# Performance work log

Measured on AMD Instinct MI355X. Metric: run time of the kernel, lower is better.

## Reference

```python
import jax, jax.numpy as jnp
import numpy as np
import math

B, T, C = 2, 2048, 1024
H = 16
D = C // H

def setup_inputs() -> dict:
    key = jax.random.key(0)
    k1, k2, k3, k4, k5 = jax.random.split(key, 5)
    scale = 0.02
    return {
        "x": jax.random.normal(k1, (B, T, C), dtype=jnp.float32),
        "w_attn": jax.random.normal(k2, (3 * C, C), dtype=jnp.float32) * scale,
        "b_attn": jax.random.normal(k3, (3 * C,), dtype=jnp.float32) * scale,
        "w_proj": jax.random.normal(k4, (C, C), dtype=jnp.float32) * scale,
        "b_proj": jax.random.normal(k5, (C,), dtype=jnp.float32) * scale,
    }

def reference(x, w_attn, b_attn, w_proj, b_proj):
    b, t, c = x.shape
    # c_attn: torch Linear -> x @ W.T + b, output [b, t, 3c]
    qkv = jnp.einsum('btc,fc->btf', x, w_attn) + b_attn
    # einops 'b t (a h d) -> a b h t d' with a=3, h=H
    qkv = qkv.reshape(b, t, 3, H, D).transpose(2, 0, 3, 1, 4)
    q, k, v = qkv[0], qkv[1], qkv[2]  # each [b, h, t, d]
    att = jnp.einsum('bhtd,bhsd->bhts', q, k) * (1.0 / math.sqrt(D))
    # causal mask: positions s > t are masked
    mask = jnp.tril(jnp.ones((t, t), dtype=bool))
    att = jnp.where(mask[None, None, :, :], att, jnp.float32(-jnp.inf))
    att = jax.nn.softmax(att, axis=-1)
    y = jnp.einsum('bhts,bhsd->bhtd', att, v)  # [b, h, t, d]
    y = y.transpose(0, 2, 1, 3).reshape(b, t, c)
    return jnp.einsum('btc,fc->btf', y, w_proj) + b_proj
```

## Files before the change

### kernel.cpp

```cpp
#include <hip/hip_runtime.h>
#include <stdint.h>

typedef unsigned short u16;
typedef __attribute__((ext_vector_type(8))) __bf16 bvec8;
typedef __attribute__((ext_vector_type(4))) float f32x4;

__device__ __forceinline__ u16 f32_to_bf16(float f) {
    uint32_t u = __float_as_uint(f);
    u += 0x7fffu + ((u >> 16) & 1u);
    return (u16)(u >> 16);
}

__device__ __forceinline__ void gl2lds16(const u16* g, u16* l) {
    void* gnc = const_cast<void*>((const void*)g);
    __builtin_amdgcn_global_load_lds(
        (__attribute__((address_space(1))) uint32_t*)gnc,
        (__attribute__((address_space(3))) uint32_t*)((void*)l),
        16, 0, 0);
}

__global__ __launch_bounds__(256) void cvt3(
    const float* __restrict__ a, int na4, const float* __restrict__ b, int nb4,
    const float* __restrict__ c, int nc4,
    u16* __restrict__ oa, u16* __restrict__ ob, u16* __restrict__ oc)
{
    int i = blockIdx.x * 256 + threadIdx.x;
    const float* src; u16* dst; int off;
    if (i < na4)             { src = a; dst = oa; off = i; }
    else if (i < na4 + nb4)  { src = b; dst = ob; off = i - na4; }
    else if (i < na4 + nb4 + nc4) { src = c; dst = oc; off = i - na4 - nb4; }
    else return;
    float4 v = ((const float4*)src)[off];
    ushort4 o;
    o.x = f32_to_bf16(v.x); o.y = f32_to_bf16(v.y);
    o.z = f32_to_bf16(v.z); o.w = f32_to_bf16(v.w);
    ((ushort4*)dst)[off] = o;
}

template <int BNt, bool OUT_BF16>
__global__ __launch_bounds__(256) void gemm_bt_bias(
    const u16* __restrict__ A, const u16* __restrict__ B,
    const float* __restrict__ bias, void* __restrict__ Cv,
    int M, int N, int K)
{
    constexpr int NT = BNt / 32;
    __shared__ __attribute__((aligned(16))) u16 As[2][128 * 32];
    __shared__ __attribute__((aligned(16))) u16 Bs[2][BNt * 32];

    const int tid = threadIdx.x, wave = tid >> 6, lane = tid & 63;
    const int col = lane & 15, quad = lane >> 4;
    const int m0 = blockIdx.y * 128, n0 = blockIdx.x * BNt;
    const int wm = (wave >> 1) * 64, wn = (wave & 1) * (BNt / 2);
    const int srow = lane >> 2, schunk = lane & 3;
    const int fs = (srow & 3) ^ ((srow >> 2) & 3);
    const int sc = (schunk ^ fs) * 8;
    const int xsw = (quad ^ (col & 3) ^ ((col >> 2) & 3)) * 8;

    const u16* Ag = A + (size_t)(m0 + wave * 32) * K;
    const u16* Bg = B + (size_t)(n0 + wave * (BNt == 128 ? 32 : 16)) * K;

    f32x4 acc[4][NT];
#pragma unroll
    for (int i = 0; i < 4; i++)
#pragma unroll
        for (int j = 0; j < NT; j++) acc[i][j] = f32x4{0.f, 0.f, 0.f, 0.f};

    auto stage = [&](int bb, int k0) {
        gl2lds16(Ag + (size_t)(srow)      * K + k0 + sc, &As[bb][(wave * 2 + 0) * 512]);
        gl2lds16(Ag + (size_t)(16 + srow) * K + k0 + sc, &As[bb][(wave * 2 + 1) * 512]);
        if constexpr (BNt == 128) {
            gl2lds16(Bg + (size_t)(srow)      * K + k0 + sc, &Bs[bb][(wave * 2 + 0) * 512]);
            gl2lds16(Bg + (size_t)(16 + srow) * K + k0 + sc, &Bs[bb][(wave * 2 + 1) * 512]);
        } else {
            gl2lds16(Bg + (size_t)(srow)      * K + k0 + sc, &Bs[bb][wave * 512]);
        }
    };

    stage(0, 0);
    const int NS = K / 32;

    for (int t = 0; t < NS; ++t) {
        const int cur = t & 1;
        if (t + 1 < NS) {
            stage(cur ^ 1, (t + 1) * 32);
            if constexpr (BNt == 128) asm volatile("s_waitcnt vmcnt(4)" ::: "memory");
            else                      asm volatile("s_waitcnt vmcnt(3)" ::: "memory");
        } else {
            asm volatile("s_waitcnt vmcnt(0)" ::: "memory");
        }
        asm volatile("s_barrier" ::: "memory");

        bvec8 af[4], bfv[NT];
#pragma unroll
        for (int mt = 0; mt < 4; mt++)  af[mt]  = *(const bvec8*)&As[cur][(wm + mt * 16 + col) * 32 + xsw];
#pragma unroll
        for (int nt = 0; nt < NT; nt++) bfv[nt] = *(const bvec8*)&Bs[cur][(wn + nt * 16 + col) * 32 + xsw];
#pragma unroll
        for (int mt = 0; mt < 4; mt++)
#pragma unroll
            for (int nt = 0; nt < NT; nt++)
                acc[mt][nt] = __builtin_amdgcn_mfma_f32_16x16x32_bf16(af[mt], bfv[nt], acc[mt][nt], 0, 0, 0);

        asm volatile("s_barrier" ::: "memory");
    }

#pragma unroll
    for (int mt = 0; mt < 4; mt++) {
#pragma unroll
        for (int r = 0; r < 4; r++) {
            const int m = m0 + wm + mt * 16 + quad * 4 + r;
#pragma unroll
            for (int nt = 0; nt < NT; nt++) {
                const int n = n0 + wn + nt * 16 + col;
                float v = acc[mt][nt][r] + bias[n];
                if (OUT_BF16) ((u16*)Cv)[(size_t)m * N + n] = f32_to_bf16(v);
                else          ((float*)Cv)[(size_t)m * N + n] = v;
            }
        }
    }
}

__global__ __launch_bounds__(256) void transpose_v(const u16* __restrict__ qkv,
                                                   u16* __restrict__ vT)
{
    __shared__ u16 Ts[64 * 74];
    const int tid = threadIdx.x;
    const int t0 = blockIdx.x * 64, h = blockIdx.y, b = blockIdx.z;
    const u16* src = qkv + (size_t)b * 2048 * 3072 + 2048 + h * 64;
#pragma unroll
    for (int k2 = 0; k2 < 2; k2++) {
        int c = k2 * 256 + tid, tl = c >> 3, ch = c & 7;
        *(uint4*)&Ts[tl * 74 + ch * 8] = *(const uint4*)(src + (size_t)(t0 + tl) * 3072 + ch * 8);
    }
    __syncthreads();
    u16* dst = vT + (size_t)((b * 16 + h) * 64) * 2048;
#pragma unroll
    for (int k2 = 0; k2 < 2; k2++) {
        int c = k2 * 256 + tid, d = c >> 3, tch = c & 7;
        u16 tmp[8];
#pragma unroll
        for (int j2 = 0; j2 < 8; j2++) tmp[j2] = Ts[(tch * 8 + j2) * 74 + d];
        *(uint4*)&dst[(size_t)d * 2048 + t0 + tch * 8] = *(const uint4*)tmp;
    }
}

__global__ __launch_bounds__(256) void attn_kernel(const u16* __restrict__ qkv,
                                                   const u16* __restrict__ vT,
                                                   u16* __restrict__ Y)
{
    __shared__ __attribute__((aligned(16))) u16 Ks[2][64 * 64];
    __shared__ __attribute__((aligned(16))) u16 Vs[2][64 * 64];

    const int tid = threadIdx.x, wave = tid >> 6, lane = tid & 63;
    const int col = lane & 15, quad = lane >> 4;

    const int g = blockIdx.x;
    const int b = g >> 4, h = g & 15;
    const int y0 = blockIdx.y & 7, s = blockIdx.y >> 3;
    const int qt = (s & 1) ? ((s & 2) ? 8 + y0 : y0)
                           : ((s & 2) ? 23 - y0 : 31 - y0);
    const int q0 = qt * 64;

    const u16* qb = qkv + (size_t)b * 2048 * 3072;
    const u16* vb = vT + (size_t)g * 64 * 2048;

    const int c0 = wave * 64 + lane, c1 = 256 + c0;
    const int r0 = c0 >> 3, p0 = c0 & 7, r1 = c1 >> 3, p1 = c1 & 7;
    const int sw0 = (p0 ^ (r0 & 7)) * 8, sw1 = (p1 ^ (r1 & 7)) * 8;
    const int tau0 = (r0 & 32) | ((r0 & 12) << 1) | ((r0 & 16) >> 2) | (r0 & 3);
    const int tau1 = (r1 & 32) | ((r1 & 12) << 1) | ((r1 & 16) >> 2) | (r1 & 3);

    const int q8 = quad * 8;
    const int qit = wave * 16 + col;
    const int qrow = wave * 16 + col;

    gl2lds16(qb + (size_t)(tau0) * 3072 + 1024 + h * 64 + sw0, &Ks[0][wave * 512]);
    gl2lds16(qb + (size_t)(tau1) * 3072 + 1024 + h * 64 + sw1, &Ks[0][2048 + wave * 512]);
    gl2lds16(vb + (size_t)r0 * 2048 + sw0, &Vs[0][wave * 512]);
    gl2lds16(vb + (size_t)r1 * 2048 + sw1, &Vs[0][2048 + wave * 512]);

    const u16* qrp = qb + (size_t)(q0 + qrow) * 3072 + h * 64;
    bvec8 qf0 = *(const bvec8*)(qrp + quad * 8);
    bvec8 qf1 = *(const bvec8*)(qrp + 32 + quad * 8);

    float l_acc = 0.f;
    f32x4 o[4];
#pragma unroll
    for (int d = 0; d < 4; d++) o[d] = f32x4{0.f, 0.f, 0.f, 0.f};

    for (int kt = 0; kt <= qt; ++kt) {
        const int cur = kt & 1;
        if (kt < qt) {
            const int s0n = (kt + 1) * 64;
            const int nb2 = cur ^ 1;
            gl2lds16(qb + (size_t)(s0n + tau0) * 3072 + 1024 + h * 64 + sw0, &Ks[nb2][wave * 512]);
            gl2lds16(qb + (size_t)(s0n + tau1) * 3072 + 1024 + h * 64 + sw1, &Ks[nb2][2048 + wave * 512]);
            gl2lds16(vb + (size_t)r0 * 2048 + s0n + sw0, &Vs[nb2][wave * 512]);
            gl2lds16(vb + (size_t)r1 * 2048 + s0n + sw1, &Vs[nb2][2048 + wave * 512]);
            asm volatile("s_waitcnt vmcnt(4)" ::: "memory");
        } else {
            asm volatile("s_waitcnt vmcnt(0)" ::: "memory");
        }
        asm volatile("s_barrier" ::: "memory");

        f32x4 sv[4];
#pragma unroll
        for (int nt = 0; nt < 4; nt++) {
            const int krow = nt * 16 + col;
            bvec8 kf0 = *(const bvec8*)&Ks[cur][krow * 64 + ((quad       ^ (krow & 7)) * 8)];
            bvec8 kf1 = *(const bvec8*)&Ks[cur][krow * 64 + (((4 + quad) ^ (krow & 7)) * 8)];
            sv[nt] = f32x4{0.f, 0.f, 0.f, 0.f};
            sv[nt] = __builtin_amdgcn_mfma_f32_16x16x32_bf16(kf0, qf0, sv[nt], 0, 0, 0);
            sv[nt] = __builtin_amdgcn_mfma_f32_16x16x32_bf16(kf1, qf1, sv[nt], 0, 0, 0);
        }

        const bool diag = (kt == qt);
        bvec8 pbv[2];
#pragma unroll
        for (int nt = 0; nt < 4; nt++) {
#pragma unroll
            for (int r = 0; r < 4; r++) {
                float p = __builtin_amdgcn_exp2f(sv[nt][r] * 0.1803368801111244f);
                const int klog = 32 * (nt >> 1) + q8 + 4 * (nt & 1) + r;
                if (diag && klog > qit) p = 0.f;
                l_acc += p;
                pbv[nt >> 1][(nt & 1) * 4 + r] = (__bf16)p;
            }
        }

#pragma unroll
        for (int ks = 0; ks < 2; ks++) {
#pragma unroll
            for (int d = 0; d < 4; d++) {
                const int vrow = d * 16 + col;
                bvec8 vf = *(const bvec8*)&Vs[cur][vrow * 64 + (((ks * 4 + quad) ^ (vrow & 7)) * 8)];
                o[d] = __builtin_amdgcn_mfma_f32_16x16x32_bf16(pbv[ks], vf, o[d], 0, 0, 0);
            }
        }
        asm volatile("s_barrier" ::: "memory");
    }

    float l = l_acc;
    l += __shfl_xor(l, 16);
    l += __shfl_xor(l, 32);
#pragma unroll
    for (int r = 0; r < 4; r++) {
        const float lr = __shfl(l, quad * 4 + r);
        const float inv = 1.0f / lr;
        const int t = q0 + wave * 16 + quad * 4 + r;
#pragma unroll
        for (int d = 0; d < 4; d++)
            Y[(size_t)(b * 2048 + t) * 1024 + h * 64 + d * 16 + col] =
                f32_to_bf16(o[d][r] * inv);
    }
}

extern "C" void kernel_launch(void* const* d_in, const int* in_sizes, int n_in,
                              void* d_out, int out_size, void* d_ws, size_t ws_size,
                              hipStream_t stream) {
    const float* x      = (const float*)d_in[0];
    const float* w_attn = (const float*)d_in[1];
    const float* b_attn = (const float*)d_in[2];
    const float* w_proj = (const float*)d_in[3];
    const float* b_proj = (const float*)d_in[4];
    float* out = (float*)d_out;

    u16* xb  = (u16*)d_ws;
    u16* wab = xb  + (size_t)4096 * 1024;
    u16* wpb = wab + (size_t)3072 * 1024;
    u16* qkv = wpb + (size_t)1024 * 1024;
    u16* y   = qkv + (size_t)4096 * 3072;
    u16* vT  = xb;

    const int na4 = 4096 * 1024 / 4, nb4 = 3072 * 1024 / 4, nc4 = 1024 * 1024 / 4;
    cvt3<<<(na4 + nb4 + nc4 + 255) / 256, 256, 0, stream>>>(
        x, na4, w_attn, nb4, w_proj, nc4, xb, wab, wpb);

    dim3 g1(3072 / 128, 4096 / 128);
    gemm_bt_bias<128, true><<<g1, 256, 0, stream>>>(xb, wab, b_attn, qkv, 4096, 3072, 1024);

    dim3 gt(32, 16, 2);
    transpose_v<<<gt, 256, 0, stream>>>(qkv, vT);

    dim3 g2(32, 32, 1);
    attn_kernel<<<g2, 256, 0, stream>>>(qkv, vT, y);

    dim3 g3(1024 / 64, 4096 / 128);
    gemm_bt_bias<64, false><<<g3, 256, 0, stream>>>(y, wpb, b_proj, out, 4096, 1024, 1024);
}
```

Before: 179.8 us.

## Halve attention block to two waves each handling 32 query rows

The attention kernel now runs with 128 threads, and each of its two waves handles two 16-row query tiles (A and B) instead of one. Every K and V fragment read from LDS feeds twice as many MFMAs, so LDS read traffic per unit of compute is halved. Each thread now issues four async global-to-LDS loads per K and V tile instead of two, and the waitcnt was raised to match. The cost is more registers per thread and fewer waves per block, which may reduce latency hiding across the barrier-synchronised loop.

```diff
diff --git a/kernel.cpp b/kernel.cpp
--- a/kernel.cpp
+++ b/kernel.cpp
@@ -144,7 +144,7 @@
     }
 }
 
-__global__ __launch_bounds__(256) void attn_kernel(const u16* __restrict__ qkv,
+__global__ __launch_bounds__(128) void attn_kernel(const u16* __restrict__ qkv,
                                                    const u16* __restrict__ vT,
                                                    u16* __restrict__ Y)
 {
@@ -164,67 +164,84 @@
     const u16* qb = qkv + (size_t)b * 2048 * 3072;
     const u16* vb = vT + (size_t)g * 64 * 2048;
 
-    const int c0 = wave * 64 + lane, c1 = 256 + c0;
-    const int r0 = c0 >> 3, p0 = c0 & 7, r1 = c1 >> 3, p1 = c1 & 7;
-    const int sw0 = (p0 ^ (r0 & 7)) * 8, sw1 = (p1 ^ (r1 & 7)) * 8;
-    const int tau0 = (r0 & 32) | ((r0 & 12) << 1) | ((r0 & 16) >> 2) | (r0 & 3);
-    const int tau1 = (r1 & 32) | ((r1 & 12) << 1) | ((r1 & 16) >> 2) | (r1 & 3);
-
-    const int q8 = quad * 8;
-    const int qit = wave * 16 + col;
-    const int qrow = wave * 16 + col;
-
-    gl2lds16(qb + (size_t)(tau0) * 3072 + 1024 + h * 64 + sw0, &Ks[0][wave * 512]);
-    gl2lds16(qb + (size_t)(tau1) * 3072 + 1024 + h * 64 + sw1, &Ks[0][2048 + wave * 512]);
-    gl2lds16(vb + (size_t)r0 * 2048 + sw0, &Vs[0][wave * 512]);
-    gl2lds16(vb + (size_t)r1 * 2048 + sw1, &Vs[0][2048 + wave * 512]);
-
-    const u16* qrp = qb + (size_t)(q0 + qrow) * 3072 + h * 64;
-    bvec8 qf0 = *(const bvec8*)(qrp + quad * 8);
-    bvec8 qf1 = *(const bvec8*)(qrp + 32 + quad * 8);
-
-    float l_acc = 0.f;
-    f32x4 o[4];
-#pragma unroll
-    for (int d = 0; d < 4; d++) o[d] = f32x4{0.f, 0.f, 0.f, 0.f};
+    int rj[4], swj[4], tj[4];
+#pragma unroll
+    for (int j = 0; j < 4; j++) {
+        const int c = j * 128 + tid, r = c >> 3, p = c & 7;
+        rj[j] = r;
+        swj[j] = (p ^ (r & 7)) * 8;
+        tj[j] = (r & 32) | ((r & 12) << 1) | ((r & 16) >> 2) | (r & 3);
+    }
+
+    auto stageK = [&](int bb, int s0) {
+#pragma unroll
+        for (int j = 0; j < 4; j++)
+            gl2lds16(qb + (size_t)(s0 + tj[j]) * 3072 + 1024 + h * 64 + swj[j],
+                     &Ks[bb][j * 1024 + wave * 512]);
+    };
+    auto stageV = [&](int bb, int s0) {
+#pragma unroll
+        for (int j = 0; j < 4; j++)
+            gl2lds16(vb + (size_t)rj[j] * 2048 + s0 + swj[j],
+                     &Vs[bb][j * 1024 + wave * 512]);
+    };
+
+    stageK(0, 0);
+    stageV(0, 0);
+
+    const int qitA = wave * 32 + col, qitB = qitA + 16;
+    const u16* qpA = qb + (size_t)(q0 + qitA) * 3072 + h * 64;
+    const u16* qpB = qpA + (size_t)16 * 3072;
+    bvec8 qfA0 = *(const bvec8*)(qpA + quad * 8);
+    bvec8 qfA1 = *(const bvec8*)(qpA + 32 + quad * 8);
+    bvec8 qfB0 = *(const bvec8*)(qpB + quad * 8);
+    bvec8 qfB1 = *(const bvec8*)(qpB + 32 + quad * 8);
+
+    float lA = 0.f, lB = 0.f;
+    f32x4 oA[4], oB[4];
+#pragma unroll
+    for (int d = 0; d < 4; d++) { oA[d] = f32x4{0.f, 0.f, 0.f, 0.f}; oB[d] = f32x4{0.f, 0.f, 0.f, 0.f}; }
 
     for (int kt = 0; kt <= qt; ++kt) {
         const int cur = kt & 1;
         if (kt < qt) {
-            const int s0n = (kt + 1) * 64;
-            const int nb2 = cur ^ 1;
-            gl2lds16(qb + (size_t)(s0n + tau0) * 3072 + 1024 + h * 64 + sw0, &Ks[nb2][wave * 512]);
-            gl2lds16(qb + (size_t)(s0n + tau1) * 3072 + 1024 + h * 64 + sw1, &Ks[nb2][2048 + wave * 512]);
-            gl2lds16(vb + (size_t)r0 * 2048 + s0n + sw0, &Vs[nb2][wave * 512]);
-            gl2lds16(vb + (size_t)r1 * 2048 + s0n + sw1, &Vs[nb2][2048 + wave * 512]);
-            asm volatile("s_waitcnt vmcnt(4)" ::: "memory");
+            stageK(cur ^ 1, (kt + 1) * 64);
+            stageV(cur ^ 1, (kt + 1) * 64);
+            asm volatile("s_waitcnt vmcnt(8)" ::: "memory");
         } else {
             asm volatile("s_waitcnt vmcnt(0)" ::: "memory");
         }
         asm volatile("s_barrier" ::: "memory");
 
-        f32x4 sv[4];
+        f32x4 svA[4], svB[4];
 #pragma unroll
         for (int nt = 0; nt < 4; nt++) {
             const int krow = nt * 16 + col;
             bvec8 kf0 = *(const bvec8*)&Ks[cur][krow * 64 + ((quad       ^ (krow & 7)) * 8)];
             bvec8 kf1 = *(const bvec8*)&Ks[cur][krow * 64 + (((4 + quad) ^ (krow & 7)) * 8)];
-            sv[nt] = f32x4{0.f, 0.f, 0.f, 0.f};
-            sv[nt] = __builtin_amdgcn_mfma_f32_16x16x32_bf16(kf0, qf0, sv[nt], 0, 0, 0);
-            sv[nt] = __builtin_amdgcn_mfma_f32_16x16x32_bf16(kf1, qf1, sv[nt], 0, 0, 0);
+            svA[nt] = f32x4{0.f, 0.f, 0.f, 0.f};
+            svA[nt] = __builtin_amdgcn_mfma_f32_16x16x32_bf16(kf0, qfA0, svA[nt], 0, 0, 0);
+            svA[nt] = __builtin_amdgcn_mfma_f32_16x16x32_bf16(kf1, qfA1, svA[nt], 0, 0, 0);
+            svB[nt] = f32x4{0.f, 0.f, 0.f, 0.f};
+            svB[nt] = __builtin_amdgcn_mfma_f32_16x16x32_bf16(kf0, qfB0, svB[nt], 0, 0, 0);
+            svB[nt] = __builtin_amdgcn_mfma_f32_16x16x32_bf16(kf1, qfB1, svB[nt], 0, 0, 0);
         }
 
         const bool diag = (kt == qt);
-        bvec8 pbv[2];
+        bvec8 pbvA[2], pbvB[2];
 #pragma unroll
         for (int nt = 0; nt < 4; nt++) {
 #pragma unroll
             for (int r = 0; r < 4; r++) {
-                float p = __builtin_amdgcn_exp2f(sv[nt][r] * 0.1803368801111244f);
-                const int klog = 32 * (nt >> 1) + q8 + 4 * (nt & 1) + r;
-                if (diag && klog > qit) p = 0.f;
-                l_acc += p;
-                pbv[nt >> 1][(nt & 1) * 4 + r] = (__bf16)p;
+                const int klog = 32 * (nt >> 1) + quad * 8 + 4 * (nt & 1) + r;
+                float pA = __builtin_amdgcn_exp2f(svA[nt][r] * 0.1803368801111244f);
+                if (diag && klog > qitA) pA = 0.f;
+                lA += pA;
+                pbvA[nt >> 1][(nt & 1) * 4 + r] = (__bf16)pA;
+                float pB = __builtin_amdgcn_exp2f(svB[nt][r] * 0.1803368801111244f);
+                if (diag && klog > qitB) pB = 0.f;
+                lB += pB;
+                pbvB[nt >> 1][(nt & 1) * 4 + r] = (__bf16)pB;
             }
         }
 
@@ -234,24 +251,42 @@
             for (int d = 0; d < 4; d++) {
                 const int vrow = d * 16 + col;
                 bvec8 vf = *(const bvec8*)&Vs[cur][vrow * 64 + (((ks * 4 + quad) ^ (vrow & 7)) * 8)];
-                o[d] = __builtin_amdgcn_mfma_f32_16x16x32_bf16(pbv[ks], vf, o[d], 0, 0, 0);
+                oA[d] = __builtin_amdgcn_mfma_f32_16x16x32_bf16(pbvA[ks], vf, oA[d], 0, 0, 0);
+                oB[d] = __builtin_amdgcn_mfma_f32_16x16x32_bf16(pbvB[ks], vf, oB[d], 0, 0, 0);
             }
         }
         asm volatile("s_barrier" ::: "memory");
     }
 
-    float l = l_acc;
-    l += __shfl_xor(l, 16);
-    l += __shfl_xor(l, 32);
-#pragma unroll
-    for (int r = 0; r < 4; r++) {
-        const float lr = __shfl(l, quad * 4 + r);
-        const float inv = 1.0f / lr;
-        const int t = q0 + wave * 16 + quad * 4 + r;
-#pragma unroll
-        for (int d = 0; d < 4; d++)
-            Y[(size_t)(b * 2048 + t) * 1024 + h * 64 + d * 16 + col] =
-                f32_to_bf16(o[d][r] * inv);
+    {
+        float l = lA;
+        l += __shfl_xor(l, 16);
+        l += __shfl_xor(l, 32);
+#pragma unroll
+        for (int r = 0; r < 4; r++) {
+            const float lr = __shfl(l, quad * 4 + r);
+            const float inv = 1.0f / lr;
+            const int t = q0 + wave * 32 + quad * 4 + r;
+#pragma unroll
+            for (int d = 0; d < 4; d++)
+                Y[(size_t)(b * 2048 + t) * 1024 + h * 64 + d * 16 + col] =
+                    f32_to_bf16(oA[d][r] * inv);
+        }
+    }
+    {
+        float l = lB;
+        l += __shfl_xor(l, 16);
+        l += __shfl_xor(l, 32);
+#pragma unroll
+        for (int r = 0; r < 4; r++) {
+            const float lr = __shfl(l, quad * 4 + r);
+            const float inv = 1.0f / lr;
+            const int t = q0 + wave * 32 + 16 + quad * 4 + r;
+#pragma unroll
+            for (int d = 0; d < 4; d++)
+                Y[(size_t)(b * 2048 + t) * 1024 + h * 64 + d * 16 + col] =
+                    f32_to_bf16(oB[d][r] * inv);
+        }
     }
 }
 
@@ -283,7 +318,7 @@
     transpose_v<<<gt, 256, 0, stream>>>(qkv, vT);
 
     dim3 g2(32, 32, 1);
-    attn_kernel<<<g2, 256, 0, stream>>>(qkv, vT, y);
+    attn_kernel<<<g2, 128, 0, stream>>>(qkv, vT, y);
 
     dim3 g3(1024 / 64, 4096 / 128);
     gemm_bt_bias<64, false><<<g3, 256, 0, stream>>>(y, wpb, b_proj, out, 4096, 1024, 1024);
```

Result: slower. 186.1 us (+3.5%).
